# Kernel tuning notes

Hardware: AMD Instinct MI355X
Metric: run time of the kernel (lower is better)

The kernel has to match this reference:

```python
import jax, jax.numpy as jnp
import numpy as np

N, R, IN, OUT = 16384, 64, 128, 128


def setup_inputs() -> dict:
    key = jax.random.key(0)
    k1, k2, k3, k4 = jax.random.split(key, 4)
    x = jax.random.normal(k1, (N, IN), dtype=jnp.float32)
    relations = jax.random.randint(k2, (N, 1), 0, R, dtype=jnp.int32)
    # kaiming_uniform_(a=sqrt(5)) on [R, in, out] -> bound = 1/sqrt(fan_in); bias uses same bound
    bound = 1.0 / np.sqrt(IN)
    w = jax.random.uniform(k3, (R, IN, OUT), dtype=jnp.float32, minval=-bound, maxval=bound)
    bias = jax.random.uniform(k4, (R, OUT), dtype=jnp.float32, minval=-bound, maxval=bound)
    return {"x": x, "relations": relations, "w": w, "bias": bias}


def reference(x, relations, w, bias):
    # Faithful math of the torch module: out[i] = x[i] @ w[relations[i,0]] + bias[relations[i,0]]
    # (original computes x.matmul(w[relations]) -> [N,1,N,out] and extracts the diagonal;
    #  this is the direct per-sample grouped GEMM form.)
    rel = relations[:, 0]                       # [N]
    w_sel = jnp.take(w, rel, axis=0)            # [N, in, out]
    out = jnp.einsum('ni,nio->no', x, w_sel)    # [N, out]
    return out + jnp.take(bias, rel, axis=0)
```

## Files before the change

### kernel.cpp

```cpp
#include <hip/hip_runtime.h>

#define N_ROWS 16384
#define R_REL  64
#define IN_D   128
#define OUT_D  128
#define BM     32
#define TPB_PRE 1024
#define TPB_G   256
#define NSLAB   16
#define HCOPIES 4
#define HSTRIDE 65

__device__ __forceinline__ float f4c(const float4& v, int i) {
  return i == 0 ? v.x : i == 1 ? v.y : i == 2 ? v.z : v.w;
}

__global__ __launch_bounds__(TPB_PRE, 1) void k_pre(const int* __restrict__ rel,
                                                    int* __restrict__ offsets,
                                                    int* __restrict__ row_idx) {
  __shared__ unsigned short srel[N_ROWS];
  __shared__ int hist[HCOPIES * HSTRIDE];
  __shared__ int cnt[R_REL];
  __shared__ int pref[R_REL + 1];
  const int t = threadIdx.x;
  const int hc = (t >> 6) & (HCOPIES - 1);

  for (int i = t; i < HCOPIES * HSTRIDE; i += TPB_PRE) hist[i] = 0;
  __syncthreads();

  int* h = &hist[hc * HSTRIDE];
  #pragma unroll
  for (int b = 0; b < N_ROWS / (TPB_PRE * 4); ++b) {
    const int idx = b * TPB_PRE + t;
    const int4 v = ((const int4*)rel)[idx];
    const int base = idx * 4;
    srel[base + 0] = (unsigned short)v.x;
    srel[base + 1] = (unsigned short)v.y;
    srel[base + 2] = (unsigned short)v.z;
    srel[base + 3] = (unsigned short)v.w;
    atomicAdd(&h[v.x], 1);
    atomicAdd(&h[v.y], 1);
    atomicAdd(&h[v.z], 1);
    atomicAdd(&h[v.w], 1);
  }
  __syncthreads();

  if (t < R_REL) {
    int v = 0;
    #pragma unroll
    for (int c = 0; c < HCOPIES; ++c) v += hist[c * HSTRIDE + t];
    #pragma unroll
    for (int d = 1; d < R_REL; d <<= 1) {
      const int u = __shfl_up(v, d, 64);
      if (t >= d) v += u;
    }
    pref[t + 1] = v;
    if (t == 0) pref[0] = 0;
  }
  __syncthreads();

  if (t < R_REL) cnt[t] = pref[t];
  if (t < R_REL + 1) offsets[t] = pref[t];
  __syncthreads();

  for (int i = t; i < N_ROWS; i += TPB_PRE) {
    const int r = srel[i];
    const int pos = atomicAdd(&cnt[r], 1);
    row_idx[pos] = i;
  }
}

__global__ __launch_bounds__(TPB_G, 4) void k_gemm(const float* __restrict__ x,
                                                   const float* __restrict__ w,
                                                   const float* __restrict__ bias,
                                                   const int* __restrict__ offsets,
                                                   const int* __restrict__ row_idx,
                                                   float* __restrict__ out) {
  __shared__ __align__(16) float xs[BM * IN_D];
  const int r = blockIdx.y;
  const int beg = offsets[r];
  const int cnt = offsets[r + 1] - beg;
  const int t  = threadIdx.x;
  const int tx = t & 15;
  const int ty = t >> 4;

  for (int tile = blockIdx.x; tile * BM < cnt; tile += NSLAB) {
    const int m0 = beg + tile * BM;
    const int rows = min(BM, cnt - tile * BM);

    {
      const int row = t & 31;
      const int q = t >> 5;
      if (row < rows) {
        const int g = row_idx[m0 + row];
        const float4* src = (const float4*)(x + (size_t)g * IN_D) + q * 4;
        float4* dst = (float4*)xs + row * 32;
        const int sw = row & 7;
        #pragma unroll
        for (int j = 0; j < 4; ++j) {
          dst[(q * 4 + j) ^ sw] = src[j];
        }
      }
    }
    __syncthreads();

    float acc[2][8];
    #pragma unroll
    for (int i = 0; i < 2; ++i)
      #pragma unroll
      for (int j = 0; j < 8; ++j) acc[i][j] = 0.f;

    const float* wp = w + (size_t)r * (IN_D * OUT_D) + tx * 8;
    const int m_a = ty * 2, m_b = ty * 2 + 1;
    const float4* xsa = (const float4*)xs + m_a * 32;
    const float4* xsb = (const float4*)xs + m_b * 32;
    const int swa = m_a & 7, swb = m_b & 7;

    #pragma unroll 4
    for (int kc = 0; kc < 32; ++kc) {
      float4 wv[4][2];
      #pragma unroll
      for (int kk = 0; kk < 4; ++kk) {
        const float4* p = (const float4*)(wp + (size_t)(kc * 4 + kk) * OUT_D);
        wv[kk][0] = p[0];
        wv[kk][1] = p[1];
      }
      const float4 xva = xsa[kc ^ swa];
      const float4 xvb = xsb[kc ^ swb];
      #pragma unroll
      for (int kk = 0; kk < 4; ++kk) {
        const float xa = f4c(xva, kk);
        const float xb = f4c(xvb, kk);
        #pragma unroll
        for (int h = 0; h < 2; ++h) {
          const float4 wq = wv[kk][h];
          acc[0][h * 4 + 0] += xa * wq.x;
          acc[0][h * 4 + 1] += xa * wq.y;
          acc[0][h * 4 + 2] += xa * wq.z;
          acc[0][h * 4 + 3] += xa * wq.w;
          acc[1][h * 4 + 0] += xb * wq.x;
          acc[1][h * 4 + 1] += xb * wq.y;
          acc[1][h * 4 + 2] += xb * wq.z;
          acc[1][h * 4 + 3] += xb * wq.w;
        }
      }
    }

    const float4* bp = (const float4*)(bias + (size_t)r * OUT_D + tx * 8);
    const float4 b0 = bp[0], b1 = bp[1];
    #pragma unroll
    for (int i = 0; i < 2; ++i) {
      const int m = ty * 2 + i;
      if (m < rows) {
        const int g = row_idx[m0 + m];
        float4* op = (float4*)(out + (size_t)g * OUT_D + tx * 8);
        float4 o0, o1;
        o0.x = acc[i][0] + b0.x; o0.y = acc[i][1] + b0.y;
        o0.z = acc[i][2] + b0.z; o0.w = acc[i][3] + b0.w;
        o1.x = acc[i][4] + b1.x; o1.y = acc[i][5] + b1.y;
        o1.z = acc[i][6] + b1.z; o1.w = acc[i][7] + b1.w;
        op[0] = o0;
        op[1] = o1;
      }
    }
    __syncthreads();
  }
}

extern "C" void kernel_launch(void* const* d_in, const int* in_sizes, int n_in,
                              void* d_out, int out_size, void* d_ws, size_t ws_size,
                              hipStream_t stream) {
  const float* x    = (const float*)d_in[0];
  const int*   rel  = (const int*)d_in[1];
  const float* w    = (const float*)d_in[2];
  const float* bias = (const float*)d_in[3];
  float* out = (float*)d_out;

  int* offsets = (int*)d_ws;
  int* row_idx = (int*)d_ws + 128;

  k_pre<<<1, TPB_PRE, 0, stream>>>(rel, offsets, row_idx);
  k_gemm<<<dim3(NSLAB, R_REL), TPB_G, 0, stream>>>(x, w, bias, offsets, row_idx, out);
}
```

Baseline: 110.0 us.

## Parallelize bucketing across relation blocks and use wave-uniform weight loads in GEMM

Result: faster. 106.2 us (-3.4%).

```diff
diff --git a/kernel.cpp b/kernel.cpp
--- a/kernel.cpp
+++ b/kernel.cpp
@@ -4,69 +4,65 @@
 #define R_REL  64
 #define IN_D   128
 #define OUT_D  128
-#define BM     32
-#define TPB_PRE 1024
-#define TPB_G   256
-#define NSLAB   16
-#define HCOPIES 4
-#define HSTRIDE 65
+#define BM     64
+#define NS     4
+#define TPB_G  256
 
 __device__ __forceinline__ float f4c(const float4& v, int i) {
   return i == 0 ? v.x : i == 1 ? v.y : i == 2 ? v.z : v.w;
 }
 
-__global__ __launch_bounds__(TPB_PRE, 1) void k_pre(const int* __restrict__ rel,
-                                                    int* __restrict__ offsets,
-                                                    int* __restrict__ row_idx) {
-  __shared__ unsigned short srel[N_ROWS];
-  __shared__ int hist[HCOPIES * HSTRIDE];
-  __shared__ int cnt[R_REL];
-  __shared__ int pref[R_REL + 1];
+__global__ __launch_bounds__(256, 4) void k_pre(const int* __restrict__ rel,
+                                                int* __restrict__ offsets,
+                                                int* __restrict__ row_idx) {
+  const int r = blockIdx.x;
   const int t = threadIdx.x;
-  const int hc = (t >> 6) & (HCOPIES - 1);
+  const int wid = t >> 6, lane = t & 63;
+  __shared__ int wsum[4];
+  __shared__ int sbase;
+  const int4* rel4 = (const int4*)rel;
 
-  for (int i = t; i < HCOPIES * HSTRIDE; i += TPB_PRE) hist[i] = 0;
+  int lt = 0;
+  for (int i = t; i < N_ROWS / 4; i += 256) {
+    const int4 v = rel4[i];
+    lt += (v.x < r) + (v.y < r) + (v.z < r) + (v.w < r);
+  }
+  #pragma unroll
+  for (int d = 32; d >= 1; d >>= 1) lt += __shfl_down(lt, d, 64);
+  if (lane == 0) wsum[wid] = lt;
   __syncthreads();
-
-  int* h = &hist[hc * HSTRIDE];
-  #pragma unroll
-  for (int b = 0; b < N_ROWS / (TPB_PRE * 4); ++b) {
-    const int idx = b * TPB_PRE + t;
-    const int4 v = ((const int4*)rel)[idx];
-    const int base = idx * 4;
-    srel[base + 0] = (unsigned short)v.x;
-    srel[base + 1] = (unsigned short)v.y;
-    srel[base + 2] = (unsigned short)v.z;
-    srel[base + 3] = (unsigned short)v.w;
-    atomicAdd(&h[v.x], 1);
-    atomicAdd(&h[v.y], 1);
-    atomicAdd(&h[v.z], 1);
-    atomicAdd(&h[v.w], 1);
+  if (t == 0) {
+    const int o = wsum[0] + wsum[1] + wsum[2] + wsum[3];
+    sbase = o;
+    offsets[r] = o;
+    if (r == R_REL - 1) offsets[R_REL] = N_ROWS;
   }
   __syncthreads();
+  int base = sbase;
 
-  if (t < R_REL) {
-    int v = 0;
+  for (int c = 0; c < 16; ++c) {
+    const int i4 = c * 256 + t;
+    const int4 v = rel4[i4];
+    const int m0 = (v.x == r), m1 = (v.y == r), m2 = (v.z == r), m3 = (v.w == r);
+    const int cnt_t = m0 + m1 + m2 + m3;
+    int incl = cnt_t;
     #pragma unroll
-    for (int c = 0; c < HCOPIES; ++c) v += hist[c * HSTRIDE + t];
-    #pragma unroll
-    for (int d = 1; d < R_REL; d <<= 1) {
-      const int u = __shfl_up(v, d, 64);
-      if (t >= d) v += u;
+    for (int d = 1; d < 64; d <<= 1) {
+      const int u = __shfl_up(incl, d, 64);
+      if (lane >= d) incl += u;
     }
-    pref[t + 1] = v;
-    if (t == 0) pref[0] = 0;
-  }
-  __syncthreads();
-
-  if (t < R_REL) cnt[t] = pref[t];
-  if (t < R_REL + 1) offsets[t] = pref[t];
-  __syncthreads();
-
-  for (int i = t; i < N_ROWS; i += TPB_PRE) {
-    const int r = srel[i];
-    const int pos = atomicAdd(&cnt[r], 1);
-    row_idx[pos] = i;
+    if (lane == 63) wsum[wid] = incl;
+    __syncthreads();
+    int wbase = 0;
+    for (int ww = 0; ww < wid; ++ww) wbase += wsum[ww];
+    int pos = base + wbase + incl - cnt_t;
+    const int row0 = i4 * 4;
+    if (m0) row_idx[pos++] = row0;
+    if (m1) row_idx[pos++] = row0 + 1;
+    if (m2) row_idx[pos++] = row0 + 2;
+    if (m3) row_idx[pos++] = row0 + 3;
+    base += wsum[0] + wsum[1] + wsum[2] + wsum[3];
+    __syncthreads();
   }
 }
 
@@ -78,90 +74,74 @@
                                                    float* __restrict__ out) {
   __shared__ __align__(16) float xs[BM * IN_D];
   const int r = blockIdx.y;
+  const int c0 = blockIdx.z * 64;
   const int beg = offsets[r];
   const int cnt = offsets[r + 1] - beg;
-  const int t  = threadIdx.x;
-  const int tx = t & 15;
-  const int ty = t >> 4;
+  if (cnt == 0) return;
+  const int t = threadIdx.x;
+  const int wq = __builtin_amdgcn_readfirstlane(t >> 6);
+  const int lane = t & 63;
+  const int cw = c0 + wq * 16;
 
-  for (int tile = blockIdx.x; tile * BM < cnt; tile += NSLAB) {
+  float bs[16];
+  #pragma unroll
+  for (int j = 0; j < 16; ++j) bs[j] = bias[(size_t)r * OUT_D + cw + j];
+
+  const float* wbase = w + (size_t)r * (IN_D * OUT_D) + cw;
+
+  for (int tile = blockIdx.x; tile * BM < cnt; tile += NS) {
     const int m0 = beg + tile * BM;
     const int rows = min(BM, cnt - tile * BM);
 
     {
-      const int row = t & 31;
-      const int q = t >> 5;
+      const int row = t & 63;
+      const int q = t >> 6;
       if (row < rows) {
         const int g = row_idx[m0 + row];
-        const float4* src = (const float4*)(x + (size_t)g * IN_D) + q * 4;
+        const float4* src = (const float4*)(x + (size_t)g * IN_D) + q * 8;
         float4* dst = (float4*)xs + row * 32;
         const int sw = row & 7;
         #pragma unroll
-        for (int j = 0; j < 4; ++j) {
-          dst[(q * 4 + j) ^ sw] = src[j];
-        }
+        for (int j = 0; j < 8; ++j) dst[(q * 8 + j) ^ sw] = src[j];
       }
     }
     __syncthreads();
 
-    float acc[2][8];
+    float acc[16];
     #pragma unroll
-    for (int i = 0; i < 2; ++i)
-      #pragma unroll
-      for (int j = 0; j < 8; ++j) acc[i][j] = 0.f;
+    for (int j = 0; j < 16; ++j) acc[j] = 0.f;
 
-    const float* wp = w + (size_t)r * (IN_D * OUT_D) + tx * 8;
-    const int m_a = ty * 2, m_b = ty * 2 + 1;
-    const float4* xsa = (const float4*)xs + m_a * 32;
-    const float4* xsb = (const float4*)xs + m_b * 32;
-    const int swa = m_a & 7, swb = m_b & 7;
+    const float4* xp = (const float4*)xs + lane * 32;
+    const int sw = lane & 7;
 
     #pragma unroll 4
     for (int kc = 0; kc < 32; ++kc) {
-      float4 wv[4][2];
+      const float4 xv = xp[kc ^ sw];
       #pragma unroll
       for (int kk = 0; kk < 4; ++kk) {
-        const float4* p = (const float4*)(wp + (size_t)(kc * 4 + kk) * OUT_D);
-        wv[kk][0] = p[0];
-        wv[kk][1] = p[1];
-      }
-      const float4 xva = xsa[kc ^ swa];
-      const float4 xvb = xsb[kc ^ swb];
-      #pragma unroll
-      for (int kk = 0; kk < 4; ++kk) {
-        const float xa = f4c(xva, kk);
-        const float xb = f4c(xvb, kk);
+        const float* wk = wbase + (size_t)(kc * 4 + kk) * OUT_D;
+        const float xk = f4c(xv, kk);
         #pragma unroll
-        for (int h = 0; h < 2; ++h) {
-          const float4 wq = wv[kk][h];
-          acc[0][h * 4 + 0] += xa * wq.x;
-          acc[0][h * 4 + 1] += xa * wq.y;
-          acc[0][h * 4 + 2] += xa * wq.z;
-          acc[0][h * 4 + 3] += xa * wq.w;
-          acc[1][h * 4 + 0] += xb * wq.x;
-          acc[1][h * 4 + 1] += xb * wq.y;
-          acc[1][h * 4 + 2] += xb * wq.z;
-          acc[1][h * 4 + 3] += xb * wq.w;
-        }
+        for (int j = 0; j < 16; ++j) acc[j] = fmaf(wk[j], xk, acc[j]);
       }
     }
 
-    const float4* bp = (const float4*)(bias + (size_t)r * OUT_D + tx * 8);
-    const float4 b0 = bp[0], b1 = bp[1];
-    #pragma unroll
-    for (int i = 0; i < 2; ++i) {
-      const int m = ty * 2 + i;
-      if (m < rows) {
-        const int g = row_idx[m0 + m];
-        float4* op = (float4*)(out + (size_t)g * OUT_D + tx * 8);
-        float4 o0, o1;
-        o0.x = acc[i][0] + b0.x; o0.y = acc[i][1] + b0.y;
-        o0.z = acc[i][2] + b0.z; o0.w = acc[i][3] + b0.w;
-        o1.x = acc[i][4] + b1.x; o1.y = acc[i][5] + b1.y;
-        o1.z = acc[i][6] + b1.z; o1.w = acc[i][7] + b1.w;
-        op[0] = o0;
-        op[1] = o1;
-      }
+    if (lane < rows) {
+      const int g = row_idx[m0 + lane];
+      float* op = out + (size_t)g * OUT_D + cw;
+      float4 o;
+      o.x = acc[0] + bs[0];  o.y = acc[1] + bs[1];
+      o.z = acc[2] + bs[2];  o.w = acc[3] + bs[3];
+      *(float4*)(op + 0) = o;
+      o.x = acc[4] + bs[4];  o.y = acc[5] + bs[5];
+      o.z = acc[6] + bs[6];  o.w = acc[7] + bs[7];
+      *(float4*)(op + 4) = o;
+      o.x = acc[8] + bs[8];  o.y = acc[9] + bs[9];
+      o.z = acc[10] + bs[10]; o.w = acc[11] + bs[11];
+      *(float4*)(op + 8) = o;
+      o.x = acc[12] + bs[12]; o.y = acc[13] + bs[13];
+      o.z = acc[14] + bs[14]; o.w = acc[15] + bs[15];
+      *(float4*)(op + 12) = o;
     }
     __syncthreads();
   }
@@ -179,6 +159,6 @@
   int* offsets = (int*)d_ws;
   int* row_idx = (int*)d_ws + 128;
 
-  k_pre<<<1, TPB_PRE, 0, stream>>>(rel, offsets, row_idx);
-  k_gemm<<<dim3(NSLAB, R_REL), TPB_G, 0, stream>>>(x, w, bias, offsets, row_idx, out);
+  k_pre<<<R_REL, 256, 0, stream>>>(rel, offsets, row_idx);
+  k_gemm<<<dim3(NS, R_REL, 2), TPB_G, 0, stream>>>(x, w, bias, offsets, row_idx, out);
 }
```
